# Kernel tuning notes

Hardware: AMD Instinct MI355X
Metric: run time of the kernel (lower is better)

Reference implementation:

```python
import jax, jax.numpy as jnp
import numpy as np


def _conv(x, w, b):
    # 'same' conv, NCHW / OIHW
    p = (w.shape[-1] - 1) // 2
    y = jax.lax.conv_general_dilated(x, w, (1, 1), [(p, p), (p, p)],
                                     dimension_numbers=('NCHW', 'OIHW', 'NCHW'))
    return y + b[None, :, None, None]


def _maxpool2(x):
    return jax.lax.reduce_window(x, -jnp.inf, jax.lax.max,
                                 (1, 1, 2, 2), (1, 1, 2, 2), 'VALID')


def setup_inputs():
    key = jax.random.key(0)
    ks = jax.random.split(key, 8)
    T, B, C, H, W = 8, 32, 1, 256, 256
    Hc = H // 4  # after two 2x2 maxpools
    s = 0.1
    return {
        "obs": jax.random.normal(ks[0], (T, B, C, H, W), jnp.float32),
        "w1": jax.random.normal(ks[1], (4, C, 5, 5), jnp.float32) * s,
        "b1": jnp.zeros((4,), jnp.float32),
        "w2": jax.random.normal(ks[2], (4, 4, 5, 5), jnp.float32) * s,
        "b2": jnp.zeros((4,), jnp.float32),
        "wx": jax.random.normal(ks[3], (32, 4, 5, 5), jnp.float32) * s,   # 4*hidden gates
        "bx": jnp.zeros((32,), jnp.float32),
        "wh": jax.random.normal(ks[4], (32, 8, 5, 5), jnp.float32) * s,
        "bh": jnp.zeros((32,), jnp.float32),
        "w_ci": jax.random.normal(ks[5], (1, 8, Hc, Hc), jnp.float32) * s,  # Hadamard peepholes
        "w_cf": jax.random.normal(ks[6], (1, 8, Hc, Hc), jnp.float32) * s,
        "w_co": jax.random.normal(ks[7], (1, 8, Hc, Hc), jnp.float32) * s,
    }


def reference(obs, w1, b1, w2, b2, wx, bx, wh, bh, w_ci, w_cf, w_co):
    T, B = obs.shape[0], obs.shape[1]
    # per-frame conv encoder, vectorized by folding frames into batch
    x = obs.reshape((T * B,) + obs.shape[2:])
    x = _maxpool2(jax.nn.relu(_conv(x, w1, b1)))
    x = _maxpool2(jax.nn.relu(_conv(x, w2, b2)))        # (T*B, 4, Hc, Hc)
    # precompute input-to-gate convs for all frames at once
    xg = _conv(x, wx, bx)                                # (T*B, 32, Hc, Hc)
    Hc = xg.shape[-1]
    xg = xg.reshape(T, B, 32, Hc, Hc)

    h0 = jnp.zeros((B, 8, Hc, Hc), jnp.float32)
    c0 = jnp.zeros((B, 8, Hc, Hc), jnp.float32)

    def step(carry, xg_t):
        h, c = carry
        g = xg_t + _conv(h, wh, bh)                      # (B, 32, Hc, Hc)
        gi, gf, gc, go = jnp.split(g, 4, axis=1)
        i = jax.nn.sigmoid(gi + c * w_ci)
        f = jax.nn.sigmoid(gf + c * w_cf)
        c_new = f * c + i * jnp.tanh(gc)
        o = jax.nn.sigmoid(go + c_new * w_co)
        h_new = o * jnp.tanh(c_new)
        return (h_new, c_new), None

    (h, c), _ = jax.lax.scan(step, (h0, c0), xg)
    return h, c
```

## Files before the change

kernel.cpp:

```cpp
#include <hip/hip_runtime.h>
#include <math.h>

typedef _Float16 f16x8 __attribute__((ext_vector_type(8)));
typedef _Float16 f16x4 __attribute__((ext_vector_type(4)));
typedef float    f32x16 __attribute__((ext_vector_type(16)));
typedef unsigned int u32;

#define DEVINL __device__ __forceinline__

DEVINL float fast_sigmoid(float x) {
    x = fminf(fmaxf(x, -30.f), 30.f);
    return 1.0f / (1.0f + __expf(-x));
}
DEVINL float fast_tanh(float x) {
    x = fminf(fmaxf(x, -15.f), 15.f);
    float e = __expf(-2.f * x);
    return (1.f - e) / (1.f + e);
}
DEVINL f16x8 f16x8_zero() {
    f16x8 v;
    #pragma unroll
    for (int j = 0; j < 8; ++j) v[j] = (_Float16)0.f;
    return v;
}

#define TKY(t) ((t) < 25 ? (t) / 5 : 2)
#define TKX(t) ((t) < 25 ? (t) % 5 : 2)

__global__ void kT_prep(const float* __restrict__ w1, const float* __restrict__ w2,
                        const float* __restrict__ wx, const float* __restrict__ wh,
                        const float* __restrict__ bx, const float* __restrict__ bh,
                        _Float16* __restrict__ wk1F, _Float16* __restrict__ w2F,
                        _Float16* __restrict__ wxF, _Float16* __restrict__ whF,
                        float* __restrict__ btot,
                        float* __restrict__ cfr, _Float16* __restrict__ hA)
{
    int t = blockIdx.x * 256 + threadIdx.x;
    int stride = gridDim.x * 256;

    for (int i = t; i < 3 * 512; i += stride) {
        int j = i & 7, l = (i >> 3) & 63, q = i >> 9;
        int g = l >> 5, m = l & 31;
        int pr = 2 * q + g, pc = j;
        float v = 0.f;
        if (m < 16) {
            int oc = m >> 2, qy = (m >> 1) & 1, qx = m & 1;
            int ky = pr - qy, kx = pc - qx;
            if ((unsigned)ky < 5u && (unsigned)kx < 5u)
                v = w1[oc * 25 + ky * 5 + kx];
        }
        wk1F[i] = (_Float16)v;
    }
    for (int i = t; i < 12 * 512; i += stride) {
        int j = i & 7, l = (i >> 3) & 63, q = i >> 9;
        int g = l >> 5, m = l & 31;
        int k = q * 16 + g * 8 + j;
        int pr = k >> 5, pc = (k >> 2) & 7, ic = k & 3;
        float v = 0.f;
        if (m < 16) {
            int oc = m >> 2, qy = (m >> 1) & 1, qx = m & 1;
            int ky = pr - qy, kx = pc - qx;
            if ((unsigned)ky < 5u && (unsigned)kx < 5u)
                v = w2[(oc * 4 + ic) * 25 + ky * 5 + kx];
        }
        w2F[i] = (_Float16)v;
    }
    for (int i = t; i < 10 * 512; i += stride) {
        int j = i & 7, l = (i >> 3) & 63, q = i >> 9;
        int g = l >> 5, m = l & 31;
        int k = q * 16 + g * 8 + j;
        int pr = k >> 5, pc = (k >> 2) & 7, ic = k & 3;
        int og = (m & 3) * 8 + (m >> 2);
        float v = (pr < 5 && pc < 5) ? wx[(og * 4 + ic) * 25 + pr * 5 + pc] : 0.f;
        wxF[i] = (_Float16)v;
    }
    for (int i = t; i < 14 * 512; i += stride) {
        int j = i & 7, l = (i >> 3) & 63, q = i >> 9;
        int g = l >> 5, m = l & 31;
        int og = (m & 3) * 8 + (m >> 2);
        int tap = 2 * q + g;
        int icj = 2 * (j & 3) + (j >> 2);
        float v = (tap < 25) ? wh[(og * 8 + icj) * 25 + tap] : 0.f;
        whF[i] = (_Float16)v;
    }
    if (t < 32) {
        int og = (t & 3) * 8 + (t >> 2);
        btot[t] = bx[og] + bh[og];
    }
    float4 z4 = make_float4(0.f, 0.f, 0.f, 0.f);
    for (int i = t; i < 262144; i += stride) ((float4*)cfr)[i] = z4;
    for (int i = t; i < 131072; i += stride) ((float4*)hA)[i]  = z4;
}

__global__ __launch_bounds__(256, 4) void k1_mfma(
    const float* __restrict__ obs, const _Float16* __restrict__ wk1F,
    const float* __restrict__ b1, _Float16* __restrict__ s1cl)
{
    __shared__ _Float16 lds[36 * 264];
    u32* ldsu = (u32*)lds;
    int tid = threadIdx.x;
    int lane = tid & 63, w = tid >> 6, g = lane >> 5;
    int yt = blockIdx.x & 7;
    int tb = blockIdx.x >> 3;
    const float* in = obs + ((size_t)tb << 16);

    f16x8 wk1[3];
    #pragma unroll
    for (int q = 0; q < 3; ++q)
        wk1[q] = *(const f16x8*)(wk1F + ((size_t)q * 64 + lane) * 8);
    float bA = b1[g], bB = b1[g + 2];

    for (int i = tid; i < 36 * 132; i += 256) ldsu[i] = 0;
    __syncthreads();
    for (int i = tid; i < 36 * 64; i += 256) {
        int r = i >> 6, c4 = i & 63;
        int gy = (yt << 5) - 2 + r;
        if ((unsigned)gy < 256u) {
            float4 v = *(const float4*)(in + (gy << 8) + (c4 << 2));
            union { _Float16 h[2]; u32 u; } p0, p1;
            p0.h[0] = (_Float16)v.x; p0.h[1] = (_Float16)v.y;
            p1.h[0] = (_Float16)v.z; p1.h[1] = (_Float16)v.w;
            int ui = r * 132 + 1 + 2 * c4;
            ldsu[ui]     = p0.u;
            ldsu[ui + 1] = p1.u;
        }
    }
    __syncthreads();

    int y0 = yt << 4;
    #pragma unroll
    for (int i = 0; i < 16; ++i) {
        int py_loc = (w << 2) + (i >> 2);
        int px0 = (i & 3) << 5;
        int n = px0 + (lane & 31);
        const u32* lp = ldsu + (2 * py_loc + g) * 132 + n;

        f32x16 acc;
        #pragma unroll
        for (int r = 0; r < 16; ++r) acc[r] = 0.f;

        #pragma unroll
        for (int q = 0; q < 3; ++q) {
            union { f16x8 v; u32 u[4]; } bb;
            const u32* p = lp + (2 * q) * 132;
            bb.u[0] = p[0]; bb.u[1] = p[1]; bb.u[2] = p[2]; bb.u[3] = p[3];
            acc = __builtin_amdgcn_mfma_f32_32x32x16_f16(wk1[q], bb.v, acc, 0, 0, 0);
        }

        float mA = fmaxf(fmaxf(fmaxf(acc[0], acc[1]), fmaxf(acc[2], acc[3])) + bA, 0.f);
        float mB = fmaxf(fmaxf(fmaxf(acc[4], acc[5]), fmaxf(acc[6], acc[7])) + bB, 0.f);

        int pix = ((y0 + py_loc) << 7) + n;
        _Float16* dst = s1cl + (((size_t)tb << 14) + pix) * 4;
        dst[g]     = (_Float16)mA;
        dst[g + 2] = (_Float16)mB;
    }
}

__global__ __launch_bounds__(256) void k2_mfma(
    const _Float16* __restrict__ s1cl, const _Float16* __restrict__ w2F,
    const float* __restrict__ b2, _Float16* __restrict__ s2cl)
{
    __shared__ _Float16 lds[20 * 136 * 4];
    int tid = threadIdx.x;
    int lane = tid & 63, w = tid >> 6, g = lane >> 5;
    int f  = blockIdx.x >> 3;
    int yt = blockIdx.x & 7;
    int y0 = yt << 3;

    f16x8 wf[12];
    #pragma unroll
    for (int q = 0; q < 12; ++q)
        wf[q] = *(const f16x8*)(w2F + ((size_t)q * 64 + lane) * 8);

    float bA = b2[g], bB = b2[g + 2];

    for (int i = tid; i < 20 * 68; i += 256) {
        int r = i / 68, u = i % 68;
        int gy = (yt << 4) - 2 + r;
        int gx = 2 * u - 2;
        f16x8 v = f16x8_zero();
        if ((unsigned)gy < 128u && (unsigned)gx < 127u)
            v = *(const f16x8*)(s1cl + ((((size_t)f << 14) + (gy << 7) + gx) << 2));
        *(f16x8*)&lds[(r * 136 + 2 * u) * 4] = v;
    }
    __syncthreads();

    #pragma unroll
    for (int i = 0; i < 4; ++i) {
        int ct = w * 4 + i;
        int ly = ct >> 1, hx = ct & 1;
        int px = hx * 32 + (lane & 31);
        int base = (2 * ly) * 1088 + (2 * px) * 8 + g * 16;

        f32x16 acc;
        #pragma unroll
        for (int r = 0; r < 16; ++r) acc[r] = 0.f;

        #pragma unroll
        for (int q = 0; q < 12; ++q) {
            f16x8 bv = *(const f16x8*)((const char*)lds + base +
                                       ((q >> 1) * 1088 + (q & 1) * 32));
            acc = __builtin_amdgcn_mfma_f32_32x32x16_f16(wf[q], bv, acc, 0, 0, 0);
        }

        float mA = fmaxf(fmaxf(fmaxf(acc[0], acc[1]), fmaxf(acc[2], acc[3])) + bA, 0.f);
        float mB = fmaxf(fmaxf(fmaxf(acc[4], acc[5]), fmaxf(acc[6], acc[7])) + bB, 0.f);

        int pix = ((y0 + ly) << 6) + px;
        _Float16* dst = s2cl + ((((size_t)f << 12) + pix) << 2);
        dst[g]     = (_Float16)mA;
        dst[g + 2] = (_Float16)mB;
    }
}

__global__ __launch_bounds__(256) void k3_mfma(
    const _Float16* __restrict__ s2cl, const _Float16* __restrict__ wxF,
    const float* __restrict__ btot, _Float16* __restrict__ xg)
{
    __shared__ _Float16 lds[12 * 72 * 4];
    int tid = threadIdx.x;
    int lane = tid & 63, w = tid >> 6, g = lane >> 5;
    int f  = blockIdx.x >> 3;
    int yt = blockIdx.x & 7;
    int y0 = yt << 3;

    f16x8 wf[10];
    #pragma unroll
    for (int q = 0; q < 10; ++q)
        wf[q] = *(const f16x8*)(wxF + ((size_t)q * 64 + lane) * 8);

    float bsel[16];
    #pragma unroll
    for (int r = 0; r < 16; ++r) {
        int row0 = (r & 3) + 8 * (r >> 2);
        bsel[r] = g ? btot[row0 + 4] : btot[row0];
    }

    for (int i = tid; i < 12 * 36; i += 256) {
        int r = i / 36, u = i % 36;
        int gy = y0 - 2 + r;
        int gx = 2 * u - 2;
        f16x8 v = f16x8_zero();
        if ((unsigned)gy < 64u && (unsigned)gx < 63u)
            v = *(const f16x8*)(s2cl + ((((size_t)f << 12) + (gy << 6) + gx) << 2));
        *(f16x8*)&lds[(r * 72 + 2 * u) * 4] = v;
    }
    __syncthreads();

    #pragma unroll
    for (int i = 0; i < 4; ++i) {
        int ct = w * 4 + i;
        int ly = ct >> 1, hx = ct & 1;
        int px = hx * 32 + (lane & 31);
        int base = ly * 576 + px * 8 + g * 16;

        f32x16 acc;
        #pragma unroll
        for (int r = 0; r < 16; ++r) acc[r] = 0.f;

        #pragma unroll
        for (int q = 0; q < 10; ++q) {
            f16x8 bv = *(const f16x8*)((const char*)lds + base +
                                       ((q >> 1) * 576 + (q & 1) * 32));
            acc = __builtin_amdgcn_mfma_f32_32x32x16_f16(wf[q], bv, acc, 0, 0, 0);
        }

        size_t tl = (size_t)f * 128 + (y0 + ly) * 2 + hx;
        f16x8 lo, hi;
        #pragma unroll
        for (int r = 0; r < 8; ++r) {
            lo[r] = (_Float16)(acc[r] + bsel[r]);
            hi[r] = (_Float16)(acc[r + 8] + bsel[r + 8]);
        }
        _Float16* dst = xg + tl * 1024 + lane * 16;
        *(f16x8*)dst       = lo;
        *(f16x8*)(dst + 8) = hi;
    }
}

__global__ __launch_bounds__(256, 4) void k4v2(
    const _Float16* __restrict__ xg_t, const _Float16* __restrict__ hprev,
    const _Float16* __restrict__ whF, float* __restrict__ cfr,
    const float* __restrict__ wci, const float* __restrict__ wcf,
    const float* __restrict__ wco, _Float16* __restrict__ hnext,
    float* __restrict__ out_hc, int last)
{
    __shared__ _Float16 lds[6 * 68 * 8];
    int tid = threadIdx.x;
    int lane = tid & 63, w = tid >> 6, g = lane >> 5;
    int b  = blockIdx.x >> 5;
    int y0 = (blockIdx.x & 31) << 1;

    int ly = w >> 1, hx = w & 1;
    int px = hx * 32 + (lane & 31);
    int pix = ((y0 + ly) << 6) + px;
    size_t tl = (size_t)b * 128 + (y0 + ly) * 2 + hx;

    const f16x8* xs = (const f16x8*)(xg_t + tl * 1024 + (size_t)lane * 16);
    f16x8 xv0 = xs[0], xv1 = xs[1];
    float4 cv = *(const float4*)(cfr + tl * 256 + lane * 4);
    float pci[4], pcf[4], pco[4];
    #pragma unroll
    for (int cc = 0; cc < 4; ++cc) {
        int ppix = ((2 * cc + g) << 12) + pix;
        pci[cc] = wci[ppix];
        pcf[cc] = wcf[ppix];
        pco[cc] = wco[ppix];
    }
    f16x8 wf[14];
    #pragma unroll
    for (int q = 0; q < 14; ++q)
        wf[q] = *(const f16x8*)(whF + ((size_t)q * 64 + lane) * 8);

    int toffs[14];
    #pragma unroll
    for (int q = 0; q < 14; ++q) {
        int t0 = 2 * q, t1 = 2 * q + 1;
        int o0 = TKY(t0) * 1088 + TKX(t0) * 16;
        int o1 = TKY(t1) * 1088 + TKX(t1) * 16;
        toffs[q] = g ? o1 : o0;
    }

    for (int i = tid; i < 6 * 68; i += 256) {
        int r = i / 68, u = i % 68;
        int gy = y0 - 2 + r;
        int gx = u - 2;
        f16x8 v = f16x8_zero();
        if ((unsigned)gy < 64u && (unsigned)gx < 64u)
            v = *(const f16x8*)(hprev + ((((size_t)b << 12) + (gy << 6) + gx) << 3));
        *(f16x8*)&lds[(r * 68 + u) * 8] = v;
    }
    __syncthreads();

    f32x16 acc;
    #pragma unroll
    for (int r = 0; r < 8; ++r) {
        acc[r]     = (float)xv0[r];
        acc[r + 8] = (float)xv1[r];
    }

    int base = ly * 1088 + px * 16;
    #pragma unroll
    for (int q = 0; q < 14; ++q) {
        f16x8 bv = *(const f16x8*)((const char*)lds + base + toffs[q]);
        acc = __builtin_amdgcn_mfma_f32_32x32x16_f16(wf[q], bv, acc, 0, 0, 0);
    }

    float cvv[4] = {cv.x, cv.y, cv.z, cv.w};
    float cn4[4];
    f16x4 hv;
    #pragma unroll
    for (int cc = 0; cc < 4; ++cc) {
        float c_old = cvv[cc];
        float i_ = fast_sigmoid(acc[4 * cc + 0] + c_old * pci[cc]);
        float f_ = fast_sigmoid(acc[4 * cc + 1] + c_old * pcf[cc]);
        float cn = f_ * c_old + i_ * fast_tanh(acc[4 * cc + 2]);
        float o_ = fast_sigmoid(acc[4 * cc + 3] + cn * pco[cc]);
        float hn = o_ * fast_tanh(cn);
        cn4[cc] = cn;
        hv[cc] = (_Float16)hn;
        if (last) {
            int ch = 2 * cc + g;
            size_t sidx = (((size_t)b * 8 + ch) << 12) + pix;
            out_hc[sidx] = hn;
            out_hc[sidx + 1048576] = cn;
        }
    }
    if (!last) {
        *(float4*)(cfr + tl * 256 + lane * 4) =
            make_float4(cn4[0], cn4[1], cn4[2], cn4[3]);
        *(f16x4*)(hnext + ((((size_t)b << 12) + pix) << 3) + 4 * g) = hv;
    }
}

extern "C" void kernel_launch(void* const* d_in, const int* in_sizes, int n_in,
                              void* d_out, int out_size, void* d_ws, size_t ws_size,
                              hipStream_t stream)
{
    const float* obs = (const float*)d_in[0];
    const float* w1  = (const float*)d_in[1];
    const float* b1  = (const float*)d_in[2];
    const float* w2  = (const float*)d_in[3];
    const float* b2  = (const float*)d_in[4];
    const float* wx  = (const float*)d_in[5];
    const float* bx  = (const float*)d_in[6];
    const float* wh  = (const float*)d_in[7];
    const float* bh  = (const float*)d_in[8];
    const float* wci = (const float*)d_in[9];
    const float* wcf = (const float*)d_in[10];
    const float* wco = (const float*)d_in[11];

    char* wsb = (char*)d_ws;
    _Float16* xg   = (_Float16*)wsb;
    _Float16* s1cl = (_Float16*)wsb;
    _Float16* s2cl = (_Float16*)(wsb + 67108864);
    _Float16* hA   = (_Float16*)(wsb + 75497472);
    _Float16* hB   = (_Float16*)(wsb + 77594624);
    float*    cfr  = (float*)(wsb + 79691776);
    _Float16* w2F  = (_Float16*)(wsb + 83886080);
    _Float16* wxF  = (_Float16*)(wsb + 83898368);
    _Float16* whF  = (_Float16*)(wsb + 83908608);
    _Float16* wk1F = (_Float16*)(wsb + 83922944);
    float*    btot = (float*)(wsb + 83927040);

    kT_prep<<<64, 256, 0, stream>>>(w1, w2, wx, wh, bx, bh,
                                    wk1F, w2F, wxF, whF, btot, cfr, hA);

    k1_mfma<<<2048, 256, 0, stream>>>(obs, wk1F, b1, s1cl);
    k2_mfma<<<2048, 256, 0, stream>>>(s1cl, w2F, b2, s2cl);
    k3_mfma<<<2048, 256, 0, stream>>>(s2cl, wxF, btot, xg);

    float* outp = (float*)d_out;
    for (int t = 0; t < 8; ++t) {
        const _Float16* hp = (t & 1) ? hB : hA;
        _Float16*       hn = (t & 1) ? hA : hB;
        k4v2<<<1024, 256, 0, stream>>>(
            xg + (size_t)t * 4194304, hp, whF, cfr,
            wci, wcf, wco, hn, outp, t == 7);
    }
}
```

Baseline: 149.0 us.

## Fuse the three encoder conv stages into one kernel with LDS halos

```diff
diff --git a/kernel.cpp b/kernel.cpp
--- a/kernel.cpp
+++ b/kernel.cpp
@@ -92,190 +92,162 @@
     for (int i = t; i < 131072; i += stride) ((float4*)hA)[i]  = z4;
 }
 
-__global__ __launch_bounds__(256, 4) void k1_mfma(
-    const float* __restrict__ obs, const _Float16* __restrict__ wk1F,
-    const float* __restrict__ b1, _Float16* __restrict__ s1cl)
+__global__ __launch_bounds__(256, 2) void k123(
+    const float* __restrict__ obs,
+    const _Float16* __restrict__ wk1F, const float* __restrict__ b1,
+    const _Float16* __restrict__ w2F, const float* __restrict__ b2,
+    const _Float16* __restrict__ wxF, const float* __restrict__ btot,
+    _Float16* __restrict__ xg)
 {
-    __shared__ _Float16 lds[36 * 264];
-    u32* ldsu = (u32*)lds;
+    __shared__ _Float16 sObs[60 * 264];
+    __shared__ _Float16 sS1[28 * 136 * 4];
+    __shared__ _Float16 sS2[12 * 72 * 4];
+    u32* obsU = (u32*)sObs;
+    u32* s1U  = (u32*)sS1;
+    u32* s2U  = (u32*)sS2;
+
     int tid = threadIdx.x;
     int lane = tid & 63, w = tid >> 6, g = lane >> 5;
-    int yt = blockIdx.x & 7;
-    int tb = blockIdx.x >> 3;
-    const float* in = obs + ((size_t)tb << 16);
-
-    f16x8 wk1[3];
-    #pragma unroll
-    for (int q = 0; q < 3; ++q)
-        wk1[q] = *(const f16x8*)(wk1F + ((size_t)q * 64 + lane) * 8);
-    float bA = b1[g], bB = b1[g + 2];
-
-    for (int i = tid; i < 36 * 132; i += 256) ldsu[i] = 0;
-    __syncthreads();
-    for (int i = tid; i < 36 * 64; i += 256) {
+    int band = blockIdx.x & 7;
+    int f = blockIdx.x >> 3;
+    int y0 = band << 3;
+    const float* in = obs + ((size_t)f << 16);
+
+    for (int i = tid; i < 60 * 132; i += 256) obsU[i] = 0;
+    for (int i = tid; i < 448; i += 256) {
+        int r = i >> 4, c = (i >> 1) & 7, half = i & 1;
+        int col = (c < 2) ? c : 128 + c;
+        s1U[r * 272 + col * 2 + half] = 0;
+    }
+    for (int i = tid; i < 192; i += 256) {
+        int r = i >> 4, c = (i >> 1) & 7, half = i & 1;
+        int col = (c < 2) ? c : 64 + c;
+        s2U[r * 144 + col * 2 + half] = 0;
+    }
+    __syncthreads();
+
+    int ob0 = (y0 << 2) - 14;
+    for (int i = tid; i < 60 * 64; i += 256) {
         int r = i >> 6, c4 = i & 63;
-        int gy = (yt << 5) - 2 + r;
+        int gy = ob0 + r;
         if ((unsigned)gy < 256u) {
             float4 v = *(const float4*)(in + (gy << 8) + (c4 << 2));
             union { _Float16 h[2]; u32 u; } p0, p1;
             p0.h[0] = (_Float16)v.x; p0.h[1] = (_Float16)v.y;
             p1.h[0] = (_Float16)v.z; p1.h[1] = (_Float16)v.w;
             int ui = r * 132 + 1 + 2 * c4;
-            ldsu[ui]     = p0.u;
-            ldsu[ui + 1] = p1.u;
-        }
-    }
-    __syncthreads();
-
-    int y0 = yt << 4;
-    #pragma unroll
-    for (int i = 0; i < 16; ++i) {
-        int py_loc = (w << 2) + (i >> 2);
-        int px0 = (i & 3) << 5;
-        int n = px0 + (lane & 31);
-        const u32* lp = ldsu + (2 * py_loc + g) * 132 + n;
-
-        f32x16 acc;
-        #pragma unroll
-        for (int r = 0; r < 16; ++r) acc[r] = 0.f;
-
-        #pragma unroll
-        for (int q = 0; q < 3; ++q) {
-            union { f16x8 v; u32 u[4]; } bb;
-            const u32* p = lp + (2 * q) * 132;
-            bb.u[0] = p[0]; bb.u[1] = p[1]; bb.u[2] = p[2]; bb.u[3] = p[3];
-            acc = __builtin_amdgcn_mfma_f32_32x32x16_f16(wk1[q], bb.v, acc, 0, 0, 0);
-        }
-
-        float mA = fmaxf(fmaxf(fmaxf(acc[0], acc[1]), fmaxf(acc[2], acc[3])) + bA, 0.f);
-        float mB = fmaxf(fmaxf(fmaxf(acc[4], acc[5]), fmaxf(acc[6], acc[7])) + bB, 0.f);
-
-        int pix = ((y0 + py_loc) << 7) + n;
-        _Float16* dst = s1cl + (((size_t)tb << 14) + pix) * 4;
-        dst[g]     = (_Float16)mA;
-        dst[g + 2] = (_Float16)mB;
-    }
-}
-
-__global__ __launch_bounds__(256) void k2_mfma(
-    const _Float16* __restrict__ s1cl, const _Float16* __restrict__ w2F,
-    const float* __restrict__ b2, _Float16* __restrict__ s2cl)
-{
-    __shared__ _Float16 lds[20 * 136 * 4];
-    int tid = threadIdx.x;
-    int lane = tid & 63, w = tid >> 6, g = lane >> 5;
-    int f  = blockIdx.x >> 3;
-    int yt = blockIdx.x & 7;
-    int y0 = yt << 3;
-
-    f16x8 wf[12];
-    #pragma unroll
-    for (int q = 0; q < 12; ++q)
-        wf[q] = *(const f16x8*)(w2F + ((size_t)q * 64 + lane) * 8);
-
-    float bA = b2[g], bB = b2[g + 2];
-
-    for (int i = tid; i < 20 * 68; i += 256) {
-        int r = i / 68, u = i % 68;
-        int gy = (yt << 4) - 2 + r;
-        int gx = 2 * u - 2;
-        f16x8 v = f16x8_zero();
-        if ((unsigned)gy < 128u && (unsigned)gx < 127u)
-            v = *(const f16x8*)(s1cl + ((((size_t)f << 14) + (gy << 7) + gx) << 2));
-        *(f16x8*)&lds[(r * 136 + 2 * u) * 4] = v;
-    }
-    __syncthreads();
-
-    #pragma unroll
-    for (int i = 0; i < 4; ++i) {
-        int ct = w * 4 + i;
-        int ly = ct >> 1, hx = ct & 1;
-        int px = hx * 32 + (lane & 31);
-        int base = (2 * ly) * 1088 + (2 * px) * 8 + g * 16;
-
-        f32x16 acc;
-        #pragma unroll
-        for (int r = 0; r < 16; ++r) acc[r] = 0.f;
-
-        #pragma unroll
-        for (int q = 0; q < 12; ++q) {
-            f16x8 bv = *(const f16x8*)((const char*)lds + base +
-                                       ((q >> 1) * 1088 + (q & 1) * 32));
-            acc = __builtin_amdgcn_mfma_f32_32x32x16_f16(wf[q], bv, acc, 0, 0, 0);
-        }
-
-        float mA = fmaxf(fmaxf(fmaxf(acc[0], acc[1]), fmaxf(acc[2], acc[3])) + bA, 0.f);
-        float mB = fmaxf(fmaxf(fmaxf(acc[4], acc[5]), fmaxf(acc[6], acc[7])) + bB, 0.f);
-
-        int pix = ((y0 + ly) << 6) + px;
-        _Float16* dst = s2cl + ((((size_t)f << 12) + pix) << 2);
-        dst[g]     = (_Float16)mA;
-        dst[g + 2] = (_Float16)mB;
-    }
-}
-
-__global__ __launch_bounds__(256) void k3_mfma(
-    const _Float16* __restrict__ s2cl, const _Float16* __restrict__ wxF,
-    const float* __restrict__ btot, _Float16* __restrict__ xg)
-{
-    __shared__ _Float16 lds[12 * 72 * 4];
-    int tid = threadIdx.x;
-    int lane = tid & 63, w = tid >> 6, g = lane >> 5;
-    int f  = blockIdx.x >> 3;
-    int yt = blockIdx.x & 7;
-    int y0 = yt << 3;
-
-    f16x8 wf[10];
-    #pragma unroll
-    for (int q = 0; q < 10; ++q)
-        wf[q] = *(const f16x8*)(wxF + ((size_t)q * 64 + lane) * 8);
-
-    float bsel[16];
-    #pragma unroll
-    for (int r = 0; r < 16; ++r) {
-        int row0 = (r & 3) + 8 * (r >> 2);
-        bsel[r] = g ? btot[row0 + 4] : btot[row0];
-    }
-
-    for (int i = tid; i < 12 * 36; i += 256) {
-        int r = i / 36, u = i % 36;
-        int gy = y0 - 2 + r;
-        int gx = 2 * u - 2;
-        f16x8 v = f16x8_zero();
-        if ((unsigned)gy < 64u && (unsigned)gx < 63u)
-            v = *(const f16x8*)(s2cl + ((((size_t)f << 12) + (gy << 6) + gx) << 2));
-        *(f16x8*)&lds[(r * 72 + 2 * u) * 4] = v;
-    }
-    __syncthreads();
-
-    #pragma unroll
-    for (int i = 0; i < 4; ++i) {
-        int ct = w * 4 + i;
-        int ly = ct >> 1, hx = ct & 1;
-        int px = hx * 32 + (lane & 31);
-        int base = ly * 576 + px * 8 + g * 16;
-
-        f32x16 acc;
-        #pragma unroll
-        for (int r = 0; r < 16; ++r) acc[r] = 0.f;
-
-        #pragma unroll
-        for (int q = 0; q < 10; ++q) {
-            f16x8 bv = *(const f16x8*)((const char*)lds + base +
-                                       ((q >> 1) * 576 + (q & 1) * 32));
-            acc = __builtin_amdgcn_mfma_f32_32x32x16_f16(wf[q], bv, acc, 0, 0, 0);
-        }
-
-        size_t tl = (size_t)f * 128 + (y0 + ly) * 2 + hx;
-        f16x8 lo, hi;
-        #pragma unroll
-        for (int r = 0; r < 8; ++r) {
-            lo[r] = (_Float16)(acc[r] + bsel[r]);
-            hi[r] = (_Float16)(acc[r + 8] + bsel[r + 8]);
-        }
-        _Float16* dst = xg + tl * 1024 + lane * 16;
-        *(f16x8*)dst       = lo;
-        *(f16x8*)(dst + 8) = hi;
+            obsU[ui] = p0.u; obsU[ui + 1] = p1.u;
+        }
+    }
+    __syncthreads();
+
+    {
+        f16x8 wk1[3];
+        #pragma unroll
+        for (int q = 0; q < 3; ++q)
+            wk1[q] = *(const f16x8*)(wk1F + ((size_t)q * 64 + lane) * 8);
+        float bA = b1[g], bB = b1[g + 2];
+        int s1base = (y0 << 1) - 6;
+        #pragma unroll
+        for (int i = 0; i < 28; ++i) {
+            int tt = w * 28 + i;
+            int s = tt >> 2;
+            int n = ((tt & 3) << 5) + (lane & 31);
+            bool valid = (unsigned)(s1base + s) < 128u;
+
+            f32x16 acc;
+            #pragma unroll
+            for (int r = 0; r < 16; ++r) acc[r] = 0.f;
+            #pragma unroll
+            for (int q = 0; q < 3; ++q) {
+                const u32* p = obsU + (2 * s + 2 * q + g) * 132 + n;
+                union { f16x8 v; u32 u[4]; } bb;
+                bb.u[0] = p[0]; bb.u[1] = p[1]; bb.u[2] = p[2]; bb.u[3] = p[3];
+                acc = __builtin_amdgcn_mfma_f32_32x32x16_f16(wk1[q], bb.v, acc, 0, 0, 0);
+            }
+            float mA = 0.f, mB = 0.f;
+            if (valid) {
+                mA = fmaxf(fmaxf(fmaxf(acc[0], acc[1]), fmaxf(acc[2], acc[3])) + bA, 0.f);
+                mB = fmaxf(fmaxf(fmaxf(acc[4], acc[5]), fmaxf(acc[6], acc[7])) + bB, 0.f);
+            }
+            sS1[((s * 136 + n + 2) << 2) + g]     = (_Float16)mA;
+            sS1[((s * 136 + n + 2) << 2) + g + 2] = (_Float16)mB;
+        }
+    }
+    __syncthreads();
+
+    {
+        f16x8 wf2[12];
+        #pragma unroll
+        for (int q = 0; q < 12; ++q)
+            wf2[q] = *(const f16x8*)(w2F + ((size_t)q * 64 + lane) * 8);
+        float bA = b2[g], bB = b2[g + 2];
+        #pragma unroll
+        for (int i = 0; i < 6; ++i) {
+            int tt = w * 6 + i;
+            int r = tt >> 1, hx = tt & 1;
+            int px = (hx << 5) + (lane & 31);
+            bool valid = (unsigned)(y0 - 2 + r) < 64u;
+
+            f32x16 acc;
+            #pragma unroll
+            for (int q = 0; q < 16; ++q) acc[q] = 0.f;
+            int base = 2 * r * 1088 + px * 16 + g * 16;
+            #pragma unroll
+            for (int q = 0; q < 12; ++q) {
+                f16x8 bv = *(const f16x8*)((const char*)sS1 + base +
+                                           ((q >> 1) * 1088 + (q & 1) * 32));
+                acc = __builtin_amdgcn_mfma_f32_32x32x16_f16(wf2[q], bv, acc, 0, 0, 0);
+            }
+            float mA = 0.f, mB = 0.f;
+            if (valid) {
+                mA = fmaxf(fmaxf(fmaxf(acc[0], acc[1]), fmaxf(acc[2], acc[3])) + bA, 0.f);
+                mB = fmaxf(fmaxf(fmaxf(acc[4], acc[5]), fmaxf(acc[6], acc[7])) + bB, 0.f);
+            }
+            sS2[((r * 72 + px + 2) << 2) + g]     = (_Float16)mA;
+            sS2[((r * 72 + px + 2) << 2) + g + 2] = (_Float16)mB;
+        }
+    }
+    __syncthreads();
+
+    {
+        f16x8 wfx[10];
+        #pragma unroll
+        for (int q = 0; q < 10; ++q)
+            wfx[q] = *(const f16x8*)(wxF + ((size_t)q * 64 + lane) * 8);
+        float bsel[16];
+        #pragma unroll
+        for (int r = 0; r < 16; ++r) {
+            int row0 = (r & 3) + 8 * (r >> 2);
+            bsel[r] = g ? btot[row0 + 4] : btot[row0];
+        }
+        #pragma unroll
+        for (int i = 0; i < 4; ++i) {
+            int tt = (w << 2) + i;
+            int ly = tt >> 1, hx = tt & 1;
+            int px = (hx << 5) + (lane & 31);
+
+            f32x16 acc;
+            #pragma unroll
+            for (int q = 0; q < 16; ++q) acc[q] = 0.f;
+            int base = ly * 576 + px * 8 + g * 16;
+            #pragma unroll
+            for (int q = 0; q < 10; ++q) {
+                f16x8 bv = *(const f16x8*)((const char*)sS2 + base +
+                                           ((q >> 1) * 576 + (q & 1) * 32));
+                acc = __builtin_amdgcn_mfma_f32_32x32x16_f16(wfx[q], bv, acc, 0, 0, 0);
+            }
+            size_t tl = (size_t)f * 128 + (y0 + ly) * 2 + hx;
+            f16x8 lo, hi;
+            #pragma unroll
+            for (int r = 0; r < 8; ++r) {
+                lo[r] = (_Float16)(acc[r] + bsel[r]);
+                hi[r] = (_Float16)(acc[r + 8] + bsel[r + 8]);
+            }
+            _Float16* dst = xg + tl * 1024 + lane * 16;
+            *(f16x8*)dst       = lo;
+            *(f16x8*)(dst + 8) = hi;
+        }
     }
 }
 
@@ -393,23 +365,19 @@
 
     char* wsb = (char*)d_ws;
     _Float16* xg   = (_Float16*)wsb;
-    _Float16* s1cl = (_Float16*)wsb;
-    _Float16* s2cl = (_Float16*)(wsb + 67108864);
-    _Float16* hA   = (_Float16*)(wsb + 75497472);
-    _Float16* hB   = (_Float16*)(wsb + 77594624);
-    float*    cfr  = (float*)(wsb + 79691776);
-    _Float16* w2F  = (_Float16*)(wsb + 83886080);
-    _Float16* wxF  = (_Float16*)(wsb + 83898368);
-    _Float16* whF  = (_Float16*)(wsb + 83908608);
-    _Float16* wk1F = (_Float16*)(wsb + 83922944);
-    float*    btot = (float*)(wsb + 83927040);
+    _Float16* hA   = (_Float16*)(wsb + 67108864);
+    _Float16* hB   = (_Float16*)(wsb + 69206016);
+    float*    cfr  = (float*)(wsb + 71303168);
+    _Float16* w2F  = (_Float16*)(wsb + 75497472);
+    _Float16* wxF  = (_Float16*)(wsb + 75509760);
+    _Float16* whF  = (_Float16*)(wsb + 75520000);
+    _Float16* wk1F = (_Float16*)(wsb + 75534336);
+    float*    btot = (float*)(wsb + 75537408);
 
     kT_prep<<<64, 256, 0, stream>>>(w1, w2, wx, wh, bx, bh,
                                     wk1F, w2F, wxF, whF, btot, cfr, hA);
 
-    k1_mfma<<<2048, 256, 0, stream>>>(obs, wk1F, b1, s1cl);
-    k2_mfma<<<2048, 256, 0, stream>>>(s1cl, w2F, b2, s2cl);
-    k3_mfma<<<2048, 256, 0, stream>>>(s2cl, wxF, btot, xg);
+    k123<<<2048, 256, 0, stream>>>(obs, wk1F, b1, w2F, b2, wxF, btot, xg);
 
     float* outp = (float*)d_out;
     for (int t = 0; t < 8; ++t) {
```

Result: slower. 154.4 us (+3.6%).

## Fuse two ConvLSTM timesteps per launch using halo recomputation in LDS

Applied to the files above, without the earlier changes.

```diff
diff --git a/kernel.cpp b/kernel.cpp
--- a/kernel.cpp
+++ b/kernel.cpp
@@ -33,7 +33,7 @@
                         _Float16* __restrict__ wk1F, _Float16* __restrict__ w2F,
                         _Float16* __restrict__ wxF, _Float16* __restrict__ whF,
                         float* __restrict__ btot,
-                        float* __restrict__ cfr, _Float16* __restrict__ hA)
+                        float* __restrict__ cfrA, _Float16* __restrict__ hA)
 {
     int t = blockIdx.x * 256 + threadIdx.x;
     int stride = gridDim.x * 256;
@@ -88,8 +88,8 @@
         btot[t] = bx[og] + bh[og];
     }
     float4 z4 = make_float4(0.f, 0.f, 0.f, 0.f);
-    for (int i = t; i < 262144; i += stride) ((float4*)cfr)[i] = z4;
-    for (int i = t; i < 131072; i += stride) ((float4*)hA)[i]  = z4;
+    for (int i = t; i < 262144; i += stride) ((float4*)cfrA)[i] = z4;
+    for (int i = t; i < 131072; i += stride) ((float4*)hA)[i]   = z4;
 }
 
 __global__ __launch_bounds__(256, 4) void k1_mfma(
@@ -257,7 +257,7 @@
 
         f32x16 acc;
         #pragma unroll
-        for (int r = 0; r < 16; ++r) acc[r] = 0.f;
+        for (int q = 0; q < 16; ++q) acc[q] = 0.f;
 
         #pragma unroll
         for (int q = 0; q < 10; ++q) {
@@ -279,35 +279,22 @@
     }
 }
 
-__global__ __launch_bounds__(256, 4) void k4v2(
-    const _Float16* __restrict__ xg_t, const _Float16* __restrict__ hprev,
-    const _Float16* __restrict__ whF, float* __restrict__ cfr,
+__global__ __launch_bounds__(256, 4) void k4p(
+    const _Float16* __restrict__ xgA, const _Float16* __restrict__ xgB,
+    const _Float16* __restrict__ hprev, _Float16* __restrict__ hnext,
+    const float* __restrict__ cin, float* __restrict__ cout,
+    const _Float16* __restrict__ whF,
     const float* __restrict__ wci, const float* __restrict__ wcf,
-    const float* __restrict__ wco, _Float16* __restrict__ hnext,
-    float* __restrict__ out_hc, int last)
-{
-    __shared__ _Float16 lds[6 * 68 * 8];
+    const float* __restrict__ wco, float* __restrict__ out_hc, int last)
+{
+    __shared__ _Float16 sHp[12 * 68 * 8];
+    __shared__ _Float16 sHt[8 * 68 * 8];
+    __shared__ float    sC[8 * 4 * 64];
     int tid = threadIdx.x;
     int lane = tid & 63, w = tid >> 6, g = lane >> 5;
-    int b  = blockIdx.x >> 5;
-    int y0 = (blockIdx.x & 31) << 1;
-
-    int ly = w >> 1, hx = w & 1;
-    int px = hx * 32 + (lane & 31);
-    int pix = ((y0 + ly) << 6) + px;
-    size_t tl = (size_t)b * 128 + (y0 + ly) * 2 + hx;
-
-    const f16x8* xs = (const f16x8*)(xg_t + tl * 1024 + (size_t)lane * 16);
-    f16x8 xv0 = xs[0], xv1 = xs[1];
-    float4 cv = *(const float4*)(cfr + tl * 256 + lane * 4);
-    float pci[4], pcf[4], pco[4];
-    #pragma unroll
-    for (int cc = 0; cc < 4; ++cc) {
-        int ppix = ((2 * cc + g) << 12) + pix;
-        pci[cc] = wci[ppix];
-        pcf[cc] = wcf[ppix];
-        pco[cc] = wco[ppix];
-    }
+    int b  = blockIdx.x >> 4;
+    int y0 = (blockIdx.x & 15) << 2;
+
     f16x8 wf[14];
     #pragma unroll
     for (int q = 0; q < 14; ++q)
@@ -322,55 +309,121 @@
         toffs[q] = g ? o1 : o0;
     }
 
-    for (int i = tid; i < 6 * 68; i += 256) {
+    u32* htU = (u32*)sHt;
+    for (int i = tid; i < 128; i += 256) {
+        int r = i >> 4, rem = i & 15;
+        int col = rem >> 2; col = (col < 2) ? col : 64 + col;
+        htU[(r * 68 + col) * 4 + (rem & 3)] = 0;
+    }
+    for (int i = tid; i < 12 * 68; i += 256) {
         int r = i / 68, u = i % 68;
-        int gy = y0 - 2 + r;
-        int gx = u - 2;
+        int gy = y0 - 4 + r, gx = u - 2;
         f16x8 v = f16x8_zero();
         if ((unsigned)gy < 64u && (unsigned)gx < 64u)
             v = *(const f16x8*)(hprev + ((((size_t)b << 12) + (gy << 6) + gx) << 3));
-        *(f16x8*)&lds[(r * 68 + u) * 8] = v;
-    }
-    __syncthreads();
-
-    f32x16 acc;
-    #pragma unroll
-    for (int r = 0; r < 8; ++r) {
-        acc[r]     = (float)xv0[r];
-        acc[r + 8] = (float)xv1[r];
-    }
-
-    int base = ly * 1088 + px * 16;
-    #pragma unroll
-    for (int q = 0; q < 14; ++q) {
-        f16x8 bv = *(const f16x8*)((const char*)lds + base + toffs[q]);
-        acc = __builtin_amdgcn_mfma_f32_32x32x16_f16(wf[q], bv, acc, 0, 0, 0);
-    }
-
-    float cvv[4] = {cv.x, cv.y, cv.z, cv.w};
-    float cn4[4];
-    f16x4 hv;
-    #pragma unroll
-    for (int cc = 0; cc < 4; ++cc) {
-        float c_old = cvv[cc];
-        float i_ = fast_sigmoid(acc[4 * cc + 0] + c_old * pci[cc]);
-        float f_ = fast_sigmoid(acc[4 * cc + 1] + c_old * pcf[cc]);
-        float cn = f_ * c_old + i_ * fast_tanh(acc[4 * cc + 2]);
-        float o_ = fast_sigmoid(acc[4 * cc + 3] + cn * pco[cc]);
-        float hn = o_ * fast_tanh(cn);
-        cn4[cc] = cn;
-        hv[cc] = (_Float16)hn;
-        if (last) {
-            int ch = 2 * cc + g;
-            size_t sidx = (((size_t)b * 8 + ch) << 12) + pix;
-            out_hc[sidx] = hn;
-            out_hc[sidx + 1048576] = cn;
-        }
-    }
-    if (!last) {
-        *(float4*)(cfr + tl * 256 + lane * 4) =
-            make_float4(cn4[0], cn4[1], cn4[2], cn4[3]);
-        *(f16x4*)(hnext + ((((size_t)b << 12) + pix) << 3) + 4 * g) = hv;
+        *(f16x8*)&sHp[(r * 68 + u) * 8] = v;
+    }
+    __syncthreads();
+
+    #pragma unroll
+    for (int i = 0; i < 4; ++i) {
+        int tt = (w << 2) + i;
+        int ry = tt >> 1, hx = tt & 1;
+        int gy = y0 - 2 + ry;
+        int px = (hx << 5) + (lane & 31);
+        f16x4 hv;
+        #pragma unroll
+        for (int j = 0; j < 4; ++j) hv[j] = (_Float16)0.f;
+
+        if ((unsigned)gy < 64u) {
+            size_t tl = (size_t)b * 128 + gy * 2 + hx;
+            const f16x8* xs = (const f16x8*)(xgA + tl * 1024 + (size_t)lane * 16);
+            f16x8 xv0 = xs[0], xv1 = xs[1];
+            float4 cv = *(const float4*)(cin + tl * 256 + lane * 4);
+
+            f32x16 acc;
+            #pragma unroll
+            for (int r = 0; r < 8; ++r) {
+                acc[r]     = (float)xv0[r];
+                acc[r + 8] = (float)xv1[r];
+            }
+            int base = ry * 1088 + px * 16;
+            #pragma unroll
+            for (int q = 0; q < 14; ++q) {
+                f16x8 bv = *(const f16x8*)((const char*)sHp + base + toffs[q]);
+                acc = __builtin_amdgcn_mfma_f32_32x32x16_f16(wf[q], bv, acc, 0, 0, 0);
+            }
+
+            float cvv[4] = {cv.x, cv.y, cv.z, cv.w};
+            int pp0 = (g << 12) + (gy << 6) + px;
+            bool keepc = (ry >= 2 && ry < 6);
+            #pragma unroll
+            for (int cc = 0; cc < 4; ++cc) {
+                int ppix = pp0 + (cc << 13);
+                float c_old = cvv[cc];
+                float i_ = fast_sigmoid(acc[4 * cc + 0] + c_old * wci[ppix]);
+                float f_ = fast_sigmoid(acc[4 * cc + 1] + c_old * wcf[ppix]);
+                float cn = f_ * c_old + i_ * fast_tanh(acc[4 * cc + 2]);
+                float o_ = fast_sigmoid(acc[4 * cc + 3] + cn * wco[ppix]);
+                hv[cc] = (_Float16)(o_ * fast_tanh(cn));
+                if (keepc)
+                    sC[((2 * cc + g) << 8) + ((ry - 2) << 6) + px] = cn;
+            }
+        }
+        *(f16x4*)&sHt[(ry * 68 + px + 2) * 8 + (g << 2)] = hv;
+    }
+    __syncthreads();
+
+    #pragma unroll
+    for (int i = 0; i < 2; ++i) {
+        int tt = (w << 1) + i;
+        int r = tt >> 1, hx = tt & 1;
+        int gy = y0 + r;
+        int px = (hx << 5) + (lane & 31);
+        size_t tl = (size_t)b * 128 + gy * 2 + hx;
+        int pix = (gy << 6) + px;
+
+        const f16x8* xs = (const f16x8*)(xgB + tl * 1024 + (size_t)lane * 16);
+        f16x8 xv0 = xs[0], xv1 = xs[1];
+        f32x16 acc;
+        #pragma unroll
+        for (int q = 0; q < 8; ++q) {
+            acc[q]     = (float)xv0[q];
+            acc[q + 8] = (float)xv1[q];
+        }
+        int base = r * 1088 + px * 16;
+        #pragma unroll
+        for (int q = 0; q < 14; ++q) {
+            f16x8 bv = *(const f16x8*)((const char*)sHt + base + toffs[q]);
+            acc = __builtin_amdgcn_mfma_f32_32x32x16_f16(wf[q], bv, acc, 0, 0, 0);
+        }
+
+        int pp0 = (g << 12) + pix;
+        float cn4[4];
+        f16x4 hv;
+        #pragma unroll
+        for (int cc = 0; cc < 4; ++cc) {
+            int ppix = pp0 + (cc << 13);
+            float c_old = sC[((2 * cc + g) << 8) + (r << 6) + px];
+            float i_ = fast_sigmoid(acc[4 * cc + 0] + c_old * wci[ppix]);
+            float f_ = fast_sigmoid(acc[4 * cc + 1] + c_old * wcf[ppix]);
+            float cn = f_ * c_old + i_ * fast_tanh(acc[4 * cc + 2]);
+            float o_ = fast_sigmoid(acc[4 * cc + 3] + cn * wco[ppix]);
+            float hn = o_ * fast_tanh(cn);
+            cn4[cc] = cn;
+            hv[cc] = (_Float16)hn;
+            if (last) {
+                int ch = 2 * cc + g;
+                size_t sidx = (((size_t)b * 8 + ch) << 12) + pix;
+                out_hc[sidx] = hn;
+                out_hc[sidx + 1048576] = cn;
+            }
+        }
+        if (!last) {
+            *(float4*)(cout + tl * 256 + lane * 4) =
+                make_float4(cn4[0], cn4[1], cn4[2], cn4[3]);
+            *(f16x4*)(hnext + ((((size_t)b << 12) + pix) << 3) + (g << 2)) = hv;
+        }
     }
 }
 
@@ -397,26 +450,29 @@
     _Float16* s2cl = (_Float16*)(wsb + 67108864);
     _Float16* hA   = (_Float16*)(wsb + 75497472);
     _Float16* hB   = (_Float16*)(wsb + 77594624);
-    float*    cfr  = (float*)(wsb + 79691776);
-    _Float16* w2F  = (_Float16*)(wsb + 83886080);
-    _Float16* wxF  = (_Float16*)(wsb + 83898368);
-    _Float16* whF  = (_Float16*)(wsb + 83908608);
-    _Float16* wk1F = (_Float16*)(wsb + 83922944);
-    float*    btot = (float*)(wsb + 83927040);
+    float*    cfrA = (float*)(wsb + 79691776);
+    float*    cfrB = (float*)(wsb + 83886080);
+    _Float16* w2F  = (_Float16*)(wsb + 88080384);
+    _Float16* wxF  = (_Float16*)(wsb + 88092672);
+    _Float16* whF  = (_Float16*)(wsb + 88102912);
+    _Float16* wk1F = (_Float16*)(wsb + 88117248);
+    float*    btot = (float*)(wsb + 88120320);
 
     kT_prep<<<64, 256, 0, stream>>>(w1, w2, wx, wh, bx, bh,
-                                    wk1F, w2F, wxF, whF, btot, cfr, hA);
+                                    wk1F, w2F, wxF, whF, btot, cfrA, hA);
 
     k1_mfma<<<2048, 256, 0, stream>>>(obs, wk1F, b1, s1cl);
     k2_mfma<<<2048, 256, 0, stream>>>(s1cl, w2F, b2, s2cl);
     k3_mfma<<<2048, 256, 0, stream>>>(s2cl, wxF, btot, xg);
 
     float* outp = (float*)d_out;
-    for (int t = 0; t < 8; ++t) {
-        const _Float16* hp = (t & 1) ? hB : hA;
-        _Float16*       hn = (t & 1) ? hA : hB;
-        k4v2<<<1024, 256, 0, stream>>>(
-            xg + (size_t)t * 4194304, hp, whF, cfr,
-            wci, wcf, wco, hn, outp, t == 7);
-    }
-}
+    const size_t XS = 4194304;
+    k4p<<<512, 256, 0, stream>>>(xg,          xg + XS,     hA, hB, cfrA, cfrB,
+                                 whF, wci, wcf, wco, outp, 0);
+    k4p<<<512, 256, 0, stream>>>(xg + 2 * XS, xg + 3 * XS, hB, hA, cfrB, cfrA,
+                                 whF, wci, wcf, wco, outp, 0);
+    k4p<<<512, 256, 0, stream>>>(xg + 4 * XS, xg + 5 * XS, hA, hB, cfrA, cfrB,
+                                 whF, wci, wcf, wco, outp, 0);
+    k4p<<<512, 256, 0, stream>>>(xg + 6 * XS, xg + 7 * XS, hB, hA, cfrB, cfrA,
+                                 whF, wci, wcf, wco, outp, 1);
+}
```

New measurement: 160.3 us. 7.5% more time.

## Fuse input-to-gate conv into recurrent LSTM step kernel, drop xg buffer

Applied to the files above, without the earlier changes.

```diff
diff --git a/kernel.cpp b/kernel.cpp
--- a/kernel.cpp
+++ b/kernel.cpp
@@ -214,79 +214,16 @@
     }
 }
 
-__global__ __launch_bounds__(256) void k3_mfma(
-    const _Float16* __restrict__ s2cl, const _Float16* __restrict__ wxF,
-    const float* __restrict__ btot, _Float16* __restrict__ xg)
-{
-    __shared__ _Float16 lds[12 * 72 * 4];
-    int tid = threadIdx.x;
-    int lane = tid & 63, w = tid >> 6, g = lane >> 5;
-    int f  = blockIdx.x >> 3;
-    int yt = blockIdx.x & 7;
-    int y0 = yt << 3;
-
-    f16x8 wf[10];
-    #pragma unroll
-    for (int q = 0; q < 10; ++q)
-        wf[q] = *(const f16x8*)(wxF + ((size_t)q * 64 + lane) * 8);
-
-    float bsel[16];
-    #pragma unroll
-    for (int r = 0; r < 16; ++r) {
-        int row0 = (r & 3) + 8 * (r >> 2);
-        bsel[r] = g ? btot[row0 + 4] : btot[row0];
-    }
-
-    for (int i = tid; i < 12 * 36; i += 256) {
-        int r = i / 36, u = i % 36;
-        int gy = y0 - 2 + r;
-        int gx = 2 * u - 2;
-        f16x8 v = f16x8_zero();
-        if ((unsigned)gy < 64u && (unsigned)gx < 63u)
-            v = *(const f16x8*)(s2cl + ((((size_t)f << 12) + (gy << 6) + gx) << 2));
-        *(f16x8*)&lds[(r * 72 + 2 * u) * 4] = v;
-    }
-    __syncthreads();
-
-    #pragma unroll
-    for (int i = 0; i < 4; ++i) {
-        int ct = w * 4 + i;
-        int ly = ct >> 1, hx = ct & 1;
-        int px = hx * 32 + (lane & 31);
-        int base = ly * 576 + px * 8 + g * 16;
-
-        f32x16 acc;
-        #pragma unroll
-        for (int r = 0; r < 16; ++r) acc[r] = 0.f;
-
-        #pragma unroll
-        for (int q = 0; q < 10; ++q) {
-            f16x8 bv = *(const f16x8*)((const char*)lds + base +
-                                       ((q >> 1) * 576 + (q & 1) * 32));
-            acc = __builtin_amdgcn_mfma_f32_32x32x16_f16(wf[q], bv, acc, 0, 0, 0);
-        }
-
-        size_t tl = (size_t)f * 128 + (y0 + ly) * 2 + hx;
-        f16x8 lo, hi;
-        #pragma unroll
-        for (int r = 0; r < 8; ++r) {
-            lo[r] = (_Float16)(acc[r] + bsel[r]);
-            hi[r] = (_Float16)(acc[r + 8] + bsel[r + 8]);
-        }
-        _Float16* dst = xg + tl * 1024 + lane * 16;
-        *(f16x8*)dst       = lo;
-        *(f16x8*)(dst + 8) = hi;
-    }
-}
-
-__global__ __launch_bounds__(256, 4) void k4v2(
-    const _Float16* __restrict__ xg_t, const _Float16* __restrict__ hprev,
-    const _Float16* __restrict__ whF, float* __restrict__ cfr,
+__global__ __launch_bounds__(256, 4) void k4x(
+    const _Float16* __restrict__ s2t, const _Float16* __restrict__ hprev,
+    const _Float16* __restrict__ wxF, const _Float16* __restrict__ whF,
+    const float* __restrict__ btot, float* __restrict__ cfr,
     const float* __restrict__ wci, const float* __restrict__ wcf,
     const float* __restrict__ wco, _Float16* __restrict__ hnext,
     float* __restrict__ out_hc, int last)
 {
-    __shared__ _Float16 lds[6 * 68 * 8];
+    __shared__ _Float16 sH[6 * 68 * 8];
+    __shared__ _Float16 sS[6 * 72 * 4];
     int tid = threadIdx.x;
     int lane = tid & 63, w = tid >> 6, g = lane >> 5;
     int b  = blockIdx.x >> 5;
@@ -297,8 +234,6 @@
     int pix = ((y0 + ly) << 6) + px;
     size_t tl = (size_t)b * 128 + (y0 + ly) * 2 + hx;
 
-    const f16x8* xs = (const f16x8*)(xg_t + tl * 1024 + (size_t)lane * 16);
-    f16x8 xv0 = xs[0], xv1 = xs[1];
     float4 cv = *(const float4*)(cfr + tl * 256 + lane * 4);
     float pci[4], pcf[4], pco[4];
     #pragma unroll
@@ -307,19 +242,6 @@
         pci[cc] = wci[ppix];
         pcf[cc] = wcf[ppix];
         pco[cc] = wco[ppix];
-    }
-    f16x8 wf[14];
-    #pragma unroll
-    for (int q = 0; q < 14; ++q)
-        wf[q] = *(const f16x8*)(whF + ((size_t)q * 64 + lane) * 8);
-
-    int toffs[14];
-    #pragma unroll
-    for (int q = 0; q < 14; ++q) {
-        int t0 = 2 * q, t1 = 2 * q + 1;
-        int o0 = TKY(t0) * 1088 + TKX(t0) * 16;
-        int o1 = TKY(t1) * 1088 + TKX(t1) * 16;
-        toffs[q] = g ? o1 : o0;
     }
 
     for (int i = tid; i < 6 * 68; i += 256) {
@@ -329,22 +251,49 @@
         f16x8 v = f16x8_zero();
         if ((unsigned)gy < 64u && (unsigned)gx < 64u)
             v = *(const f16x8*)(hprev + ((((size_t)b << 12) + (gy << 6) + gx) << 3));
-        *(f16x8*)&lds[(r * 68 + u) * 8] = v;
+        *(f16x8*)&sH[(r * 68 + u) * 8] = v;
+    }
+    for (int i = tid; i < 6 * 36; i += 256) {
+        int r = i / 36, u = i % 36;
+        int gy = y0 - 2 + r;
+        int gx = 2 * u - 2;
+        f16x8 v = f16x8_zero();
+        if ((unsigned)gy < 64u && (unsigned)gx < 63u)
+            v = *(const f16x8*)(s2t + ((((size_t)b << 12) + (gy << 6) + gx) << 2));
+        *(f16x8*)&sS[(r * 72 + 2 * u) * 4] = v;
     }
     __syncthreads();
 
     f32x16 acc;
     #pragma unroll
-    for (int r = 0; r < 8; ++r) {
-        acc[r]     = (float)xv0[r];
-        acc[r + 8] = (float)xv1[r];
-    }
-
-    int base = ly * 1088 + px * 16;
-    #pragma unroll
-    for (int q = 0; q < 14; ++q) {
-        f16x8 bv = *(const f16x8*)((const char*)lds + base + toffs[q]);
-        acc = __builtin_amdgcn_mfma_f32_32x32x16_f16(wf[q], bv, acc, 0, 0, 0);
+    for (int r = 0; r < 16; ++r) {
+        int row0 = (r & 3) + 8 * (r >> 2);
+        acc[r] = g ? btot[row0 + 4] : btot[row0];
+    }
+
+    {
+        int baseS = ly * 576 + px * 8 + g * 16;
+        #pragma unroll
+        for (int q = 0; q < 10; ++q) {
+            f16x8 wv = *(const f16x8*)(wxF + ((size_t)q * 64 + lane) * 8);
+            f16x8 bv = *(const f16x8*)((const char*)sS + baseS +
+                                       ((q >> 1) * 576 + (q & 1) * 32));
+            acc = __builtin_amdgcn_mfma_f32_32x32x16_f16(wv, bv, acc, 0, 0, 0);
+        }
+    }
+
+    {
+        int baseH = ly * 1088 + px * 16;
+        #pragma unroll
+        for (int q = 0; q < 14; ++q) {
+            int t0 = 2 * q, t1 = 2 * q + 1;
+            int o0 = TKY(t0) * 1088 + TKX(t0) * 16;
+            int o1 = TKY(t1) * 1088 + TKX(t1) * 16;
+            int toff = g ? o1 : o0;
+            f16x8 wv = *(const f16x8*)(whF + ((size_t)q * 64 + lane) * 8);
+            f16x8 bv = *(const f16x8*)((const char*)sH + baseH + toff);
+            acc = __builtin_amdgcn_mfma_f32_32x32x16_f16(wv, bv, acc, 0, 0, 0);
+        }
     }
 
     float cvv[4] = {cv.x, cv.y, cv.z, cv.w};
@@ -392,31 +341,29 @@
     const float* wco = (const float*)d_in[11];
 
     char* wsb = (char*)d_ws;
-    _Float16* xg   = (_Float16*)wsb;
     _Float16* s1cl = (_Float16*)wsb;
-    _Float16* s2cl = (_Float16*)(wsb + 67108864);
-    _Float16* hA   = (_Float16*)(wsb + 75497472);
-    _Float16* hB   = (_Float16*)(wsb + 77594624);
-    float*    cfr  = (float*)(wsb + 79691776);
-    _Float16* w2F  = (_Float16*)(wsb + 83886080);
-    _Float16* wxF  = (_Float16*)(wsb + 83898368);
-    _Float16* whF  = (_Float16*)(wsb + 83908608);
-    _Float16* wk1F = (_Float16*)(wsb + 83922944);
-    float*    btot = (float*)(wsb + 83927040);
+    _Float16* s2cl = (_Float16*)(wsb + 33554432);
+    _Float16* hA   = (_Float16*)(wsb + 41943040);
+    _Float16* hB   = (_Float16*)(wsb + 44040192);
+    float*    cfr  = (float*)(wsb + 46137344);
+    _Float16* w2F  = (_Float16*)(wsb + 50331648);
+    _Float16* wxF  = (_Float16*)(wsb + 50343936);
+    _Float16* whF  = (_Float16*)(wsb + 50354176);
+    _Float16* wk1F = (_Float16*)(wsb + 50368512);
+    float*    btot = (float*)(wsb + 50371584);
 
     kT_prep<<<64, 256, 0, stream>>>(w1, w2, wx, wh, bx, bh,
                                     wk1F, w2F, wxF, whF, btot, cfr, hA);
 
     k1_mfma<<<2048, 256, 0, stream>>>(obs, wk1F, b1, s1cl);
     k2_mfma<<<2048, 256, 0, stream>>>(s1cl, w2F, b2, s2cl);
-    k3_mfma<<<2048, 256, 0, stream>>>(s2cl, wxF, btot, xg);
 
     float* outp = (float*)d_out;
     for (int t = 0; t < 8; ++t) {
         const _Float16* hp = (t & 1) ? hB : hA;
         _Float16*       hn = (t & 1) ? hA : hB;
-        k4v2<<<1024, 256, 0, stream>>>(
-            xg + (size_t)t * 4194304, hp, whF, cfr,
+        k4x<<<1024, 256, 0, stream>>>(
+            s2cl + (size_t)t * 524288, hp, wxF, whF, btot, cfr,
             wci, wcf, wco, hn, outp, t == 7);
     }
 }
```

Result: faster. 138.1 us (-7.3%).
